# Kernel optimization log

Hardware: AMD Instinct MI355X
Metric: run time of the kernel (lower is better)

## Reference

```python
import jax, jax.numpy as jnp
import numpy as np
import math

D_MODEL = 1024
NHEAD = 16
NUM_CLUSTERS = 32
L, N, S = 2048, 2, 2048
LN_EPS = 1e-5


def setup_inputs() -> dict:
    key = jax.random.key(0)
    ks = jax.random.split(key, 16)
    E = D_MODEL
    s = 1.0 / math.sqrt(E)
    cq = jax.random.normal(ks[0], (NUM_CLUSTERS, E), jnp.float32)
    cq = cq / jnp.linalg.norm(cq, axis=1, keepdims=True)
    ck = jax.random.normal(ks[1], (NUM_CLUSTERS, E), jnp.float32)
    ck = ck / jnp.linalg.norm(ck, axis=1, keepdims=True)
    return {
        "query": jax.random.normal(ks[2], (L, N, E), jnp.float32),
        "key": jax.random.normal(ks[3], (S, N, E), jnp.float32),
        "value": jax.random.normal(ks[4], (S, N, E), jnp.float32),
        "Wq": jax.random.uniform(ks[5], (E, E), jnp.float32, -s, s),
        "bq": jax.random.uniform(ks[6], (E,), jnp.float32, -s, s),
        "Wk": jax.random.uniform(ks[7], (E, E), jnp.float32, -s, s),
        "bk": jax.random.uniform(ks[8], (E,), jnp.float32, -s, s),
        "Wv": jax.random.uniform(ks[9], (E, E), jnp.float32, -s, s),
        "bv": jax.random.uniform(ks[10], (E,), jnp.float32, -s, s),
        "Wo": jax.random.uniform(ks[11], (E, E), jnp.float32, -s, s),
        "bo": jax.random.uniform(ks[12], (E,), jnp.float32, -s, s),
        "centroids_q": cq,
        "centroids_k": ck,
        "ln_gamma": jnp.ones((E,), jnp.float32),
        "ln_beta": jnp.zeros((E,), jnp.float32),
    }


def _assign(x, centroids):
    # spherical k-means assignment: argmax cosine similarity
    xn = x / jnp.clip(jnp.linalg.norm(x, axis=-1, keepdims=True), 1e-12)
    return jnp.argmax(xn @ centroids.T, axis=-1)


def reference(query, key, value, Wq, bq, Wk, bk, Wv, bv, Wo, bo,
              centroids_q, centroids_k, ln_gamma, ln_beta):
    Lq, Nb, E = query.shape
    Sk = key.shape[0]
    H, dh = NHEAD, E // NHEAD

    Q = query @ Wq.T + bq            # [L,N,E]
    K = key @ Wk.T + bk              # [S,N,E]
    V = value @ Wv.T + bv            # [S,N,E]

    Qb = jnp.transpose(Q, (1, 0, 2))  # [N,L,E]
    Kb = jnp.transpose(K, (1, 0, 2))  # [N,S,E]
    Vb = jnp.transpose(V, (1, 0, 2))  # [N,S,E]

    q_clusters = _assign(Qb, centroids_q)  # [N,L] int
    k_clusters = _assign(Kb, centroids_k)  # [N,S] int
    # bipartite cluster-equality mask, broadcast over heads
    mask = q_clusters[:, :, None] == k_clusters[:, None, :]  # [N,L,S]

    Qh = Qb.reshape(Nb, Lq, H, dh)
    Kh = Kb.reshape(Nb, Sk, H, dh)
    Vh = Vb.reshape(Nb, Sk, H, dh)

    scores = jnp.einsum('nlhd,nshd->nhls', Qh, Kh) / math.sqrt(dh)
    scores = jnp.where(mask[:, None, :, :], scores, -jnp.inf)
    attn = jax.nn.softmax(scores, axis=-1)  # dropout = identity (eval)

    ctx = jnp.einsum('nhls,nshd->nlhd', attn, Vh).reshape(Nb, Lq, E)
    out = ctx @ Wo.T + bo                     # [N,L,E]
    out = jnp.transpose(out, (1, 0, 2))       # [L,N,E]

    res = query + out
    mu = jnp.mean(res, axis=-1, keepdims=True)
    var = jnp.mean(jnp.square(res - mu), axis=-1, keepdims=True)
    return (res - mu) / jnp.sqrt(var + LN_EPS) * ln_gamma + ln_beta
```

## Files before the change

### kernel.cpp

```cpp
#include <hip/hip_runtime.h>
#include <stdint.h>

#define L_SEQ 2048
#define S_SEQ 2048
#define NB 2
#define EMB 1024
#define NH 16
#define DH 64
#define NC 32
#define MROWS 4096

typedef __bf16 bf16x8 __attribute__((ext_vector_type(8)));
typedef float f32x4 __attribute__((ext_vector_type(4)));

__device__ __forceinline__ float bf2f(unsigned short u) {
  return __builtin_bit_cast(float, (uint32_t)u << 16);
}
__device__ __forceinline__ unsigned short f2bf(float f) {
  uint32_t u = __builtin_bit_cast(uint32_t, f);
  return (unsigned short)((u + 0x7FFFu + ((u >> 16) & 1u)) >> 16);
}

#if defined(__has_builtin) && __has_builtin(__builtin_amdgcn_global_load_lds)
#define GLOAD_LDS(gp, lp)                                            \
  __builtin_amdgcn_global_load_lds(                                  \
      (const __attribute__((address_space(1))) void*)(gp),           \
      (__attribute__((address_space(3))) void*)(lp), 16, 0, 0)
#else
#define GLOAD_LDS(gp, lp) do { *(uint4*)(lp) = *(const uint4*)(gp); } while (0)
#endif

__global__ void __launch_bounds__(256) conv_f2bf_kernel(
    const float* __restrict__ src, unsigned short* __restrict__ dst, int n8)
{
  int id = blockIdx.x * 256 + threadIdx.x;
  if (id >= n8) return;
  const float4* s = (const float4*)src + (size_t)id * 2;
  float4 a0 = s[0], a1 = s[1];
  uint4 u;
  u.x = (uint32_t)f2bf(a0.x) | ((uint32_t)f2bf(a0.y) << 16);
  u.y = (uint32_t)f2bf(a0.z) | ((uint32_t)f2bf(a0.w) << 16);
  u.z = (uint32_t)f2bf(a1.x) | ((uint32_t)f2bf(a1.y) << 16);
  u.w = (uint32_t)f2bf(a1.z) | ((uint32_t)f2bf(a1.w) << 16);
  ((uint4*)dst)[id] = u;
}

__global__ void __launch_bounds__(256) gemm_bt_mfma(
    const unsigned short* __restrict__ A, const unsigned short* __restrict__ B,
    const float* __restrict__ bias,
    float* __restrict__ outF, unsigned short* __restrict__ outB)
{
  __shared__ __align__(16) unsigned short As[128][32];
  __shared__ __align__(16) unsigned short Bs[128][32];
  const int K = EMB;
  int tid = threadIdx.x;
  int m0 = blockIdx.y * 128, n0 = blockIdx.x * 128;
  int wave = tid >> 6, lane = tid & 63;
  int wm = (wave >> 1) * 64, wn = (wave & 1) * 64;

  f32x4 zero = {0.f, 0.f, 0.f, 0.f};
  f32x4 acc[4][4];
#pragma unroll
  for (int mi = 0; mi < 4; mi++)
#pragma unroll
    for (int ni = 0; ni < 4; ni++) acc[mi][ni] = zero;

  int fr = lane & 15, fk = (lane >> 4) * 8;

  for (int k0 = 0; k0 < K; k0 += 32) {
    __syncthreads();
#pragma unroll
    for (int it = 0; it < 2; it++) {
      int ch = tid + it * 256;
      int row = ch >> 2, kk = (ch & 3) * 8;
      GLOAD_LDS(A + (size_t)(m0 + row) * K + k0 + kk, &As[row][kk]);
      GLOAD_LDS(B + (size_t)(n0 + row) * K + k0 + kk, &Bs[row][kk]);
    }
    __syncthreads();
    bf16x8 af[4], bfr[4];
#pragma unroll
    for (int i = 0; i < 4; i++) af[i] = *(const bf16x8*)(&As[wm + i * 16 + fr][fk]);
#pragma unroll
    for (int i = 0; i < 4; i++) bfr[i] = *(const bf16x8*)(&Bs[wn + i * 16 + fr][fk]);
#pragma unroll
    for (int mi = 0; mi < 4; mi++)
#pragma unroll
      for (int ni = 0; ni < 4; ni++)
        acc[mi][ni] = __builtin_amdgcn_mfma_f32_16x16x32_bf16(af[mi], bfr[ni], acc[mi][ni], 0, 0, 0);
  }

#pragma unroll
  for (int ni = 0; ni < 4; ni++) {
    int col = n0 + wn + ni * 16 + (lane & 15);
    float bv = bias[col];
#pragma unroll
    for (int mi = 0; mi < 4; mi++) {
#pragma unroll
      for (int r = 0; r < 4; r++) {
        int row = m0 + wm + mi * 16 + (lane >> 4) * 4 + r;
        float v = acc[mi][ni][r] + bv;
        if (outF) outF[(size_t)row * EMB + col] = v;
        else outB[(size_t)row * EMB + col] = f2bf(v);
      }
    }
  }
}

__global__ void __launch_bounds__(256) prep_wc_kernel(
    const float* __restrict__ W, const float* __restrict__ bias,
    const float* __restrict__ cent,
    double* __restrict__ WcT, double* __restrict__ bd)
{
  int k = blockIdx.x;
  int tid = threadIdx.x;
  int c = tid & 31, g = tid >> 5;
  __shared__ double red[8][32];
  double s = 0.0;
  for (int e = g * 128; e < (g + 1) * 128; e++)
    s += (double)W[(size_t)e * EMB + k] * (double)cent[(size_t)c * EMB + e];
  red[g][c] = s;
  __syncthreads();
  if (tid < 32) {
    double t = 0.0;
#pragma unroll
    for (int gg = 0; gg < 8; gg++) t += red[gg][tid];
    WcT[(size_t)k * NC + tid] = t;
  }
  if (k == 0) {
    __syncthreads();
    double s2 = 0.0;
    for (int e = g * 128; e < (g + 1) * 128; e++)
      s2 += (double)bias[e] * (double)cent[(size_t)c * EMB + e];
    red[g][c] = s2;
    __syncthreads();
    if (tid < 32) {
      double t = 0.0;
#pragma unroll
      for (int gg = 0; gg < 8; gg++) t += red[gg][tid];
      bd[tid] = t;
    }
  }
}

__global__ void __launch_bounds__(256, 2) assign2_kernel(
    const float* __restrict__ Xq, const double* __restrict__ WcTq, const double* __restrict__ bdq,
    int* __restrict__ qcl, int* __restrict__ qcnt,
    const float* __restrict__ Xk, const double* __restrict__ WcTk, const double* __restrict__ bdk,
    int* __restrict__ kcl, int* __restrict__ kcnt)
{
  const float* X; const double* WcT; const double* bd; int* cluster; int* count;
  if (blockIdx.y == 0) { X = Xq; WcT = WcTq; bd = bdq; cluster = qcl; count = qcnt; }
  else                 { X = Xk; WcT = WcTk; bd = bdk; cluster = kcl; count = kcnt; }

  int r0 = blockIdx.x * 16;
  int tid = threadIdx.x;
  int c = tid & 31, g = tid >> 5;

  __shared__ __align__(16) double Ws[64][32];
  __shared__ __align__(16) double Xd[16][64];

  double aAe = 0, aAo = 0, aBe = 0, aBo = 0;

  for (int k0 = 0; k0 < EMB; k0 += 64) {
    __syncthreads();
#pragma unroll
    for (int it = 0; it < 8; it++) {
      int idx = it * 256 + tid;
      ((double*)Ws)[idx] = WcT[(size_t)k0 * NC + idx];
    }
#pragma unroll
    for (int it = 0; it < 2; it++) {
      int idx = it * 256 + tid;
      int r = idx >> 5, kp = idx & 31;
      float2 xv = *(const float2*)(X + (size_t)(r0 + r) * EMB + k0 + kp * 2);
      double2 xd; xd.x = (double)xv.x; xd.y = (double)xv.y;
      *(double2*)(&Xd[r][kp * 2]) = xd;
    }
    __syncthreads();
#pragma unroll
    for (int kk = 0; kk < 64; kk += 2) {
      double w0 = Ws[kk][c], w1 = Ws[kk + 1][c];
      double2 xa = *(const double2*)(&Xd[g * 2][kk]);
      double2 xb = *(const double2*)(&Xd[g * 2 + 1][kk]);
      aAe += xa.x * w0; aAo += xa.y * w1;
      aBe += xb.x * w0; aBo += xb.y * w1;
    }
  }

  double dA = (aAe + aAo) + bd[c];
  double dB = (aBe + aBo) + bd[c];

  double bvA = dA; int biA = c;
  double bvB = dB; int biB = c;
#pragma unroll
  for (int off = 1; off < 32; off <<= 1) {
    double ovA = __shfl_xor(bvA, off, 64); int oiA = __shfl_xor(biA, off, 64);
    if (ovA > bvA || (ovA == bvA && oiA < biA)) { bvA = ovA; biA = oiA; }
    double ovB = __shfl_xor(bvB, off, 64); int oiB = __shfl_xor(biB, off, 64);
    if (ovB > bvB || (ovB == bvB && oiB < biB)) { bvB = ovB; biB = oiB; }
  }
  if (c == 0) {
    int rowA = r0 + g * 2, rowB = rowA + 1;
    cluster[rowA] = biA; atomicAdd(&count[(rowA & 1) * NC + biA], 1);
    cluster[rowB] = biB; atomicAdd(&count[(rowB & 1) * NC + biB], 1);
  }
}

__global__ void scan_kernel(const int* __restrict__ qcount, const int* __restrict__ kcount,
                            int* __restrict__ qoff, int* __restrict__ koff)
{
  int tid = threadIdx.x;
  if (tid < 2) {
    int run = 0;
    for (int c = 0; c < NC; c++) { qoff[tid * NC + c] = run; run += qcount[tid * NC + c]; }
  } else if (tid < 4) {
    int n = tid - 2, run = 0;
    for (int c = 0; c < NC; c++) { koff[n * NC + c] = run; run += kcount[n * NC + c]; }
  }
}

__global__ void __launch_bounds__(256) scatter_kernel(
    const int* __restrict__ q_cluster, const int* __restrict__ k_cluster,
    const int* __restrict__ qoff, const int* __restrict__ koff,
    int* __restrict__ qfill, int* __restrict__ kfill,
    int* __restrict__ qlist, int* __restrict__ klist)
{
  int id = blockIdx.x * 256 + threadIdx.x;
  if (id < MROWS) {
    int row = id, n = row & 1, l = row >> 1, c = q_cluster[row];
    int pos = atomicAdd(&qfill[n * NC + c], 1);
    qlist[n * L_SEQ + qoff[n * NC + c] + pos] = l;
  } else {
    int row = id - MROWS, n = row & 1, s = row >> 1, c = k_cluster[row];
    int pos = atomicAdd(&kfill[n * NC + c], 1);
    klist[n * S_SEQ + koff[n * NC + c] + pos] = s;
  }
}

__global__ void __launch_bounds__(256) attn_bucket(
    const unsigned short* __restrict__ Qb, const unsigned short* __restrict__ Kb,
    const unsigned short* __restrict__ Vb,
    const int* __restrict__ qcount, const int* __restrict__ qoff, const int* __restrict__ qlist,
    const int* __restrict__ kcount, const int* __restrict__ koff, const int* __restrict__ klist,
    unsigned short* __restrict__ ctx)
{
  int c = blockIdx.x, h = blockIdx.y, n = blockIdx.z;
  int Sc = kcount[n * NC + c], k0base = koff[n * NC + c];
  int Lc = qcount[n * NC + c], q0 = qoff[n * NC + c];
  int tid = threadIdx.x, wave = tid >> 6, lane = tid & 63;
  int lg = lane >> 4, lq = lane & 15;

  __shared__ __align__(16) unsigned short Ks[64][64];
  __shared__ __align__(16) unsigned short Vts[64][64];
  __shared__ __align__(16) unsigned short Pts[4][16][64];
  __shared__ int rb[64];

  if (Sc == 0) {
    for (int qi = wave; qi < Lc; qi += 4) {
      int l = qlist[n * L_SEQ + q0 + qi];
      ctx[((size_t)(n * L_SEQ + l)) * EMB + h * DH + lane] = 0;
    }
    return;
  }

  const int* kl = klist + n * S_SEQ + k0base;
  const int* ql = qlist + n * L_SEQ + q0;
  f32x4 zero = {0.f, 0.f, 0.f, 0.f};

  for (int qb = 0; qb < Lc; qb += 64) {
    int qq = qb + wave * 16 + lq;
    int qqc = qq < Lc ? qq : Lc - 1;
    int lrow = ql[qqc];
    const unsigned short* qp = Qb + ((size_t)(lrow * NB + n)) * EMB + h * DH;
    bf16x8 qf0 = *(const bf16x8*)(qp + lg * 8);
    bf16x8 qf1 = *(const bf16x8*)(qp + 32 + lg * 8);

    f32x4 acc[4];
#pragma unroll
    for (int di = 0; di < 4; di++) acc[di] = zero;
    float m = -3.0e38f, lsum = 0.f;

    for (int kc = 0; kc < Sc; kc += 64) {
      __syncthreads();
      if (tid < 64) {
        int jj = kc + tid; if (jj >= Sc) jj = Sc - 1;
        rb[tid] = (kl[jj] * NB + n) * EMB + h * DH;
      }
      __syncthreads();
#pragma unroll
      for (int it = 0; it < 2; it++) {
        int p = it * 256 + tid;
        {
          int row = p >> 3, seg = p & 7;
          uint4 u = *(const uint4*)(Kb + rb[row] + seg * 8);
          *(uint4*)(&Ks[row][(seg * 8) ^ ((row & 7) << 3)]) = u;
        }
        {
          int d = p & 63, kg = p >> 6;
          unsigned short v0 = Vb[rb[kg * 8 + 0] + d], v1 = Vb[rb[kg * 8 + 1] + d];
          unsigned short v2 = Vb[rb[kg * 8 + 2] + d], v3 = Vb[rb[kg * 8 + 3] + d];
          unsigned short v4 = Vb[rb[kg * 8 + 4] + d], v5 = Vb[rb[kg * 8 + 5] + d];
          unsigned short v6 = Vb[rb[kg * 8 + 6] + d], v7 = Vb[rb[kg * 8 + 7] + d];
          uint4 u;
          u.x = (uint32_t)v0 | ((uint32_t)v1 << 16);
          u.y = (uint32_t)v2 | ((uint32_t)v3 << 16);
          u.z = (uint32_t)v4 | ((uint32_t)v5 << 16);
          u.w = (uint32_t)v6 | ((uint32_t)v7 << 16);
          *(uint4*)(&Vts[d][(kg * 8) ^ ((d & 7) << 3)]) = u;
        }
      }
      __syncthreads();

      f32x4 st[4];
#pragma unroll
      for (int ni = 0; ni < 4; ni++) st[ni] = zero;
#pragma unroll
      for (int ni = 0; ni < 4; ni++) {
        int row = ni * 16 + lq;
        bf16x8 kf0 = *(const bf16x8*)(&Ks[row][(lg * 8) ^ ((row & 7) << 3)]);
        bf16x8 kf1 = *(const bf16x8*)(&Ks[row][(32 + lg * 8) ^ ((row & 7) << 3)]);
        st[ni] = __builtin_amdgcn_mfma_f32_16x16x32_bf16(kf0, qf0, st[ni], 0, 0, 0);
        st[ni] = __builtin_amdgcn_mfma_f32_16x16x32_bf16(kf1, qf1, st[ni], 0, 0, 0);
      }

      int lim = Sc - kc;
      float cm = -3.0e38f;
#pragma unroll
      for (int ni = 0; ni < 4; ni++) {
        st[ni] = st[ni] * 0.125f;
#pragma unroll
        for (int r = 0; r < 4; r++) cm = fmaxf(cm, st[ni][r]);
      }
      cm = fmaxf(cm, __shfl_xor(cm, 16, 64));
      cm = fmaxf(cm, __shfl_xor(cm, 32, 64));
      float mn = fmaxf(m, cm);
      float fac = __expf(m - mn);
      m = mn;
      lsum *= fac;
#pragma unroll
      for (int di = 0; di < 4; di++) acc[di] = acc[di] * fac;

#pragma unroll
      for (int ni = 0; ni < 4; ni++) {
        int kloc = ni * 16 + lg * 4;
        float p0 = (kloc + 0 < lim) ? __expf(st[ni][0] - mn) : 0.f;
        float p1 = (kloc + 1 < lim) ? __expf(st[ni][1] - mn) : 0.f;
        float p2 = (kloc + 2 < lim) ? __expf(st[ni][2] - mn) : 0.f;
        float p3 = (kloc + 3 < lim) ? __expf(st[ni][3] - mn) : 0.f;
        unsigned short b0 = f2bf(p0), b1 = f2bf(p1), b2 = f2bf(p2), b3 = f2bf(p3);
        lsum += bf2f(b0) + bf2f(b1) + bf2f(b2) + bf2f(b3);
        ushort4 u4; u4.x = b0; u4.y = b1; u4.z = b2; u4.w = b3;
        *(ushort4*)(&Pts[wave][lq][kloc ^ ((lq & 7) << 3)]) = u4;
      }

#pragma unroll
      for (int ks = 0; ks < 2; ks++) {
        bf16x8 pf = *(const bf16x8*)(&Pts[wave][lq][(ks * 32 + lg * 8) ^ ((lq & 7) << 3)]);
#pragma unroll
        for (int di = 0; di < 4; di++) {
          int row = di * 16 + lq;
          bf16x8 vf = *(const bf16x8*)(&Vts[row][(ks * 32 + lg * 8) ^ ((row & 7) << 3)]);
          acc[di] = __builtin_amdgcn_mfma_f32_16x16x32_bf16(vf, pf, acc[di], 0, 0, 0);
        }
      }
    }

    lsum += __shfl_xor(lsum, 16, 64);
    lsum += __shfl_xor(lsum, 32, 64);
    float rinv = 1.f / lsum;
    if (qq < Lc) {
      unsigned short* op = ctx + ((size_t)(n * L_SEQ + lrow)) * EMB + h * DH;
#pragma unroll
      for (int di = 0; di < 4; di++) {
        ushort4 o;
        o.x = f2bf(acc[di][0] * rinv);
        o.y = f2bf(acc[di][1] * rinv);
        o.z = f2bf(acc[di][2] * rinv);
        o.w = f2bf(acc[di][3] * rinv);
        *(ushort4*)(op + di * 16 + lg * 4) = o;
      }
    }
  }
}

__global__ void __launch_bounds__(256) ln_kernel(
    const float* __restrict__ proj, const float* __restrict__ query,
    const float* __restrict__ gamma, const float* __restrict__ beta,
    float* __restrict__ out)
{
  int r = blockIdx.x;
  int l = r >> 1, n = r & 1;
  int tid = threadIdx.x, wave = tid >> 6, lane = tid & 63;
  float4 p = *(const float4*)(proj + ((size_t)(n * L_SEQ + l)) * EMB + tid * 4);
  float4 qu = *(const float4*)(query + (size_t)r * EMB + tid * 4);
  float res[4] = { p.x + qu.x, p.y + qu.y, p.z + qu.z, p.w + qu.w };
  float s1 = res[0] + res[1] + res[2] + res[3];
  float s2 = res[0] * res[0] + res[1] * res[1] + res[2] * res[2] + res[3] * res[3];
#pragma unroll
  for (int off = 32; off; off >>= 1) {
    s1 += __shfl_xor(s1, off, 64);
    s2 += __shfl_xor(s2, off, 64);
  }
  __shared__ float a1[4], a2[4];
  if (lane == 0) { a1[wave] = s1; a2[wave] = s2; }
  __syncthreads();
  float t1 = a1[0] + a1[1] + a1[2] + a1[3];
  float t2 = a2[0] + a2[1] + a2[2] + a2[3];
  float mu = t1 * (1.f / EMB);
  float var = fmaxf(t2 * (1.f / EMB) - mu * mu, 0.f);
  float rstd = 1.f / sqrtf(var + 1e-5f);
  float4 gu = *(const float4*)(gamma + tid * 4);
  float4 bu = *(const float4*)(beta + tid * 4);
  float4 o;
  o.x = (res[0] - mu) * rstd * gu.x + bu.x;
  o.y = (res[1] - mu) * rstd * gu.y + bu.y;
  o.z = (res[2] - mu) * rstd * gu.z + bu.z;
  o.w = (res[3] - mu) * rstd * gu.w + bu.w;
  *(float4*)(out + (size_t)r * EMB + tid * 4) = o;
}

extern "C" void kernel_launch(void* const* d_in, const int* in_sizes, int n_in,
                              void* d_out, int out_size, void* d_ws, size_t ws_size,
                              hipStream_t stream) {
  const float* query = (const float*)d_in[0];
  const float* key   = (const float*)d_in[1];
  const float* value = (const float*)d_in[2];
  const float* Wq = (const float*)d_in[3];
  const float* bq = (const float*)d_in[4];
  const float* Wk = (const float*)d_in[5];
  const float* bk = (const float*)d_in[6];
  const float* Wv = (const float*)d_in[7];
  const float* bv = (const float*)d_in[8];
  const float* Wo = (const float*)d_in[9];
  const float* bo = (const float*)d_in[10];
  const float* cq = (const float*)d_in[11];
  const float* ck = (const float*)d_in[12];
  const float* gamma = (const float*)d_in[13];
  const float* beta  = (const float*)d_in[14];
  float* out = (float*)d_out;

  const size_t MB_EL = (size_t)MROWS * EMB;

  int* q_cluster = (int*)d_ws;
  int* k_cluster = q_cluster + MROWS;
  int* qcount = k_cluster + MROWS;
  int* kcount = qcount + 64;
  int* qoff   = kcount + 64;
  int* koff   = qoff + 64;
  int* qfill  = koff + 64;
  int* kfill  = qfill + 64;
  int* qlist  = kfill + 64;
  int* klist  = qlist + MROWS;
  double* Wcq = (double*)(klist + MROWS);
  double* Wck = Wcq + (size_t)NC * EMB;
  double* bdq = Wck + (size_t)NC * EMB;
  double* bdk = bdq + NC;
  unsigned short* Qb  = (unsigned short*)(bdk + NC);
  unsigned short* Kb  = Qb + MB_EL;
  unsigned short* Vb  = Kb + MB_EL;
  unsigned short* ctx = Vb + MB_EL;
  unsigned short* wbf = ctx + MB_EL;
  unsigned short* xbf = ctx;
  float* proj = (float*)Qb;

  const int W8 = (EMB * EMB) / 8;
  const int X8 = (int)(MB_EL / 8);

  hipMemsetAsync(qcount, 0, 6 * 64 * sizeof(int), stream);

  prep_wc_kernel<<<EMB, 256, 0, stream>>>(Wq, bq, cq, Wcq, bdq);
  prep_wc_kernel<<<EMB, 256, 0, stream>>>(Wk, bk, ck, Wck, bdk);

  dim3 gg(EMB / 128, MROWS / 128);
  conv_f2bf_kernel<<<W8 / 256, 256, 0, stream>>>(Wq, wbf, W8);
  conv_f2bf_kernel<<<X8 / 256, 256, 0, stream>>>(query, xbf, X8);
  gemm_bt_mfma<<<gg, 256, 0, stream>>>(xbf, wbf, bq, nullptr, Qb);

  conv_f2bf_kernel<<<W8 / 256, 256, 0, stream>>>(Wk, wbf, W8);
  conv_f2bf_kernel<<<X8 / 256, 256, 0, stream>>>(key, xbf, X8);
  gemm_bt_mfma<<<gg, 256, 0, stream>>>(xbf, wbf, bk, nullptr, Kb);

  conv_f2bf_kernel<<<W8 / 256, 256, 0, stream>>>(Wv, wbf, W8);
  conv_f2bf_kernel<<<X8 / 256, 256, 0, stream>>>(value, xbf, X8);
  gemm_bt_mfma<<<gg, 256, 0, stream>>>(xbf, wbf, bv, nullptr, Vb);

  assign2_kernel<<<dim3(MROWS / 16, 2), 256, 0, stream>>>(
      query, Wcq, bdq, q_cluster, qcount,
      key,   Wck, bdk, k_cluster, kcount);

  scan_kernel<<<1, 64, 0, stream>>>(qcount, kcount, qoff, koff);
  scatter_kernel<<<(2 * MROWS) / 256, 256, 0, stream>>>(q_cluster, k_cluster, qoff, koff,
                                                        qfill, kfill, qlist, klist);
  attn_bucket<<<dim3(NC, NH, NB), 256, 0, stream>>>(Qb, Kb, Vb, qcount, qoff, qlist,
                                                    kcount, koff, klist, ctx);

  conv_f2bf_kernel<<<W8 / 256, 256, 0, stream>>>(Wo, wbf, W8);
  gemm_bt_mfma<<<gg, 256, 0, stream>>>(ctx, wbf, bo, proj, nullptr);
  ln_kernel<<<MROWS, 256, 0, stream>>>(proj, query, gamma, beta, out);
}
```

Before: 408.1 us.

## Split centroid-weight precompute into coalesced partial sums plus reduction

```diff
diff --git a/kernel.cpp b/kernel.cpp
--- a/kernel.cpp
+++ b/kernel.cpp
@@ -106,39 +106,71 @@
   }
 }
 
-__global__ void __launch_bounds__(256) prep_wc_kernel(
-    const float* __restrict__ W, const float* __restrict__ bias,
-    const float* __restrict__ cent,
-    double* __restrict__ WcT, double* __restrict__ bd)
-{
-  int k = blockIdx.x;
+__global__ void __launch_bounds__(256) prep_partial_kernel(
+    const float* __restrict__ Wq_, const float* __restrict__ cq_,
+    const float* __restrict__ Wk_, const float* __restrict__ ck_,
+    double* __restrict__ partQ, double* __restrict__ partK)
+{
+  const float* W; const float* cent; double* part;
+  if (blockIdx.z == 0) { W = Wq_; cent = cq_; part = partQ; }
+  else                 { W = Wk_; cent = ck_; part = partK; }
+  int tid = threadIdx.x;
+  int k = (blockIdx.y << 6) | (tid & 63);
+  int cbase = __builtin_amdgcn_readfirstlane(tid >> 6) * 8;
+  int e0 = blockIdx.x << 6;
+
+  double acc[8];
+#pragma unroll
+  for (int j = 0; j < 8; j++) acc[j] = 0.0;
+
+#pragma unroll 2
+  for (int e = 0; e < 64; e++) {
+    double w = (double)W[(size_t)(e0 + e) * EMB + k];
+#pragma unroll
+    for (int j = 0; j < 8; j++)
+      acc[j] += w * (double)cent[(size_t)(cbase + j) * EMB + e0 + e];
+  }
+#pragma unroll
+  for (int j = 0; j < 8; j++)
+    part[((size_t)blockIdx.x * NC + cbase + j) * EMB + k] = acc[j];
+}
+
+__global__ void __launch_bounds__(256) prep_reduce_kernel(
+    const double* __restrict__ partQ, const double* __restrict__ partK,
+    double* __restrict__ WcTq, double* __restrict__ WcTk)
+{
+  int id = blockIdx.x * 256 + threadIdx.x;
+  const double* part; double* WcT; int local;
+  if (id < NC * EMB) { part = partQ; WcT = WcTq; local = id; }
+  else               { part = partK; WcT = WcTk; local = id - NC * EMB; }
+  int c = local >> 10, k = local & 1023;
+  double s = 0.0;
+  for (int es = 0; es < 16; es++)
+    s += part[((size_t)es * NC + c) * EMB + k];
+  WcT[(size_t)k * NC + c] = s;
+}
+
+__global__ void __launch_bounds__(256) prep_bd_kernel(
+    const float* __restrict__ bq_, const float* __restrict__ cq_,
+    const float* __restrict__ bk_, const float* __restrict__ ck_,
+    double* __restrict__ bdq, double* __restrict__ bdk)
+{
+  const float* bias; const float* cent; double* bd;
+  if (blockIdx.x == 0) { bias = bq_; cent = cq_; bd = bdq; }
+  else                 { bias = bk_; cent = ck_; bd = bdk; }
   int tid = threadIdx.x;
   int c = tid & 31, g = tid >> 5;
   __shared__ double red[8][32];
-  double s = 0.0;
+  double s2 = 0.0;
   for (int e = g * 128; e < (g + 1) * 128; e++)
-    s += (double)W[(size_t)e * EMB + k] * (double)cent[(size_t)c * EMB + e];
-  red[g][c] = s;
+    s2 += (double)bias[e] * (double)cent[(size_t)c * EMB + e];
+  red[g][c] = s2;
   __syncthreads();
   if (tid < 32) {
     double t = 0.0;
 #pragma unroll
     for (int gg = 0; gg < 8; gg++) t += red[gg][tid];
-    WcT[(size_t)k * NC + tid] = t;
-  }
-  if (k == 0) {
-    __syncthreads();
-    double s2 = 0.0;
-    for (int e = g * 128; e < (g + 1) * 128; e++)
-      s2 += (double)bias[e] * (double)cent[(size_t)c * EMB + e];
-    red[g][c] = s2;
-    __syncthreads();
-    if (tid < 32) {
-      double t = 0.0;
-#pragma unroll
-      for (int gg = 0; gg < 8; gg++) t += red[gg][tid];
-      bd[tid] = t;
-    }
+    bd[tid] = t;
   }
 }
 
@@ -462,14 +494,17 @@
   unsigned short* wbf = ctx + MB_EL;
   unsigned short* xbf = ctx;
   float* proj = (float*)Qb;
+  double* partQ = (double*)Qb;
+  double* partK = partQ + (size_t)16 * NC * EMB;
 
   const int W8 = (EMB * EMB) / 8;
   const int X8 = (int)(MB_EL / 8);
 
   hipMemsetAsync(qcount, 0, 6 * 64 * sizeof(int), stream);
 
-  prep_wc_kernel<<<EMB, 256, 0, stream>>>(Wq, bq, cq, Wcq, bdq);
-  prep_wc_kernel<<<EMB, 256, 0, stream>>>(Wk, bk, ck, Wck, bdk);
+  prep_partial_kernel<<<dim3(16, 16, 2), 256, 0, stream>>>(Wq, cq, Wk, ck, partQ, partK);
+  prep_reduce_kernel<<<(2 * NC * EMB) / 256, 256, 0, stream>>>(partQ, partK, Wcq, Wck);
+  prep_bd_kernel<<<2, 256, 0, stream>>>(bq, cq, bk, ck, bdq, bdk);
 
   dim3 gg(EMB / 128, MROWS / 128);
   conv_f2bf_kernel<<<W8 / 256, 256, 0, stream>>>(Wq, wbf, W8);
```

Result: faster. 369.8 us (-9.4%).
